# Performance work log

Measured on AMD Instinct MI355X. Metric: run time of the kernel, lower is better.

## Reference

```python
import jax, jax.numpy as jnp
import numpy as np

B, S, D = 2, 2048, 2048
H, HKV, HD = 32, 8, 64
G = H // HKV  # num_key_value_groups


def setup_inputs() -> dict:
    key = jax.random.key(0)
    ks = jax.random.split(key, 9)
    sc = 0.02
    return {
        "x": jax.random.normal(ks[0], (B, S, D), jnp.float32),
        "wq": jax.random.normal(ks[1], (H * HD, D), jnp.float32) * sc,
        "bq": jax.random.normal(ks[2], (H * HD,), jnp.float32) * sc,
        "wk": jax.random.normal(ks[3], (HKV * HD, D), jnp.float32) * sc,
        "bk": jax.random.normal(ks[4], (HKV * HD,), jnp.float32) * sc,
        "wv": jax.random.normal(ks[5], (HKV * HD, D), jnp.float32) * sc,
        "bv": jax.random.normal(ks[6], (HKV * HD,), jnp.float32) * sc,
        "wo": jax.random.normal(ks[7], (D, H * HD), jnp.float32) * sc,
        "bo": jax.random.normal(ks[8], (D,), jnp.float32) * sc,
    }


def reference(x, wq, bq, wk, bk, wv, bv, wo, bo):
    b, s, _ = x.shape
    # fused-QKV-style projections (nn.Linear: x @ W.T + b)
    q = (jnp.einsum("bsd,ed->bse", x, wq) + bq).reshape(b, s, H, HD)
    k = (jnp.einsum("bsd,ed->bse", x, wk) + bk).reshape(b, s, HKV, HD)
    v = (jnp.einsum("bsd,ed->bse", x, wv) + bv).reshape(b, s, HKV, HD)
    # (B, Hkv, G, S, hd): grouped query heads share a KV head — same math as
    # repeat_kv (expand+flatten) without materializing the expanded KV tensor
    q = q.transpose(0, 2, 1, 3).reshape(b, HKV, G, s, HD)
    k = k.transpose(0, 2, 1, 3)  # (B, Hkv, S, hd)
    v = v.transpose(0, 2, 1, 3)
    scale = 1.0 / jnp.sqrt(jnp.asarray(HD, x.dtype))
    scores = jnp.einsum("bkgqd,bktd->bkgqt", q, k) * scale  # (B,Hkv,G,S,S)
    causal = jnp.tril(jnp.ones((s, s), bool))
    scores = jnp.where(causal, scores, jnp.asarray(-jnp.inf, scores.dtype))
    probs = jax.nn.softmax(scores, axis=-1)
    o = jnp.einsum("bkgqt,bktd->bkgqd", probs, v)  # (B,Hkv,G,S,hd)
    o = o.reshape(b, H, s, HD).transpose(0, 2, 1, 3).reshape(b, s, H * HD)
    return jnp.einsum("bse,de->bsd", o, wo) + bo
```

## Files before the change

kernel.cpp:

```cpp
#include <hip/hip_runtime.h>
#include <hip/hip_bf16.h>
#include <cmath>

#define B_   2
#define S_   2048
#define D_   2048
#define H_   32
#define HKV_ 8
#define HD_  64

using bf16 = __hip_bfloat16;
typedef __bf16    bf16x8 __attribute__((ext_vector_type(8)));
typedef float     floatx4 __attribute__((ext_vector_type(4)));
typedef _Float16  half4 __attribute__((ext_vector_type(4)));

#if __has_builtin(__builtin_amdgcn_exp2f)
#define EXP2(x) __builtin_amdgcn_exp2f(x)
#else
#define EXP2(x) exp2f(x)
#endif

#define QSCALE 0.18033688011112042f

__device__ inline void async16(const void* g, void* l) {
  __builtin_amdgcn_global_load_lds(
      (const __attribute__((address_space(1))) void*)g,
      (__attribute__((address_space(3))) void*)l, 16, 0, 0);
}

#define MFMA32B(a, b, c) __builtin_amdgcn_mfma_f32_16x16x32_bf16((a), (b), (c), 0, 0, 0)
#define MFMA16H(a, b, c) __builtin_amdgcn_mfma_f32_16x16x16f16((a), (b), (c), 0, 0, 0)

__global__ void f2b_all(const float* __restrict__ x,  const float* __restrict__ wq,
                        const float* __restrict__ wk, const float* __restrict__ wv,
                        const float* __restrict__ wo,
                        bf16* __restrict__ xb,  bf16* __restrict__ wqb,
                        bf16* __restrict__ wkb, bf16* __restrict__ wvb,
                        bf16* __restrict__ wob) {
  const int i = blockIdx.x * blockDim.x + threadIdx.x;
  const float* src; bf16* dst; int off; float scale = 1.0f;
  if (i < 1048576)      { src = x;  dst = xb;  off = 0; }
  else if (i < 1572864) { src = wq; dst = wqb; off = 1048576; scale = QSCALE; }
  else if (i < 1703936) { src = wk; dst = wkb; off = 1572864; }
  else if (i < 1835008) { src = wv; dst = wvb; off = 1703936; }
  else                  { src = wo; dst = wob; off = 1835008; }
  const int j = i - off;
  float4 a  = ((const float4*)src)[2 * j];
  float4 b2 = ((const float4*)src)[2 * j + 1];
  alignas(16) bf16 t[8];
  t[0] = __float2bfloat16(a.x * scale);  t[1] = __float2bfloat16(a.y * scale);
  t[2] = __float2bfloat16(a.z * scale);  t[3] = __float2bfloat16(a.w * scale);
  t[4] = __float2bfloat16(b2.x * scale); t[5] = __float2bfloat16(b2.y * scale);
  t[6] = __float2bfloat16(b2.z * scale); t[7] = __float2bfloat16(b2.w * scale);
  ((uint4*)dst)[j] = *(const uint4*)t;
}

template <int MODE, typename OutT>
__device__ inline void gemm_body(const bf16* __restrict__ Ag, const bf16* __restrict__ Bg,
                                 const float* __restrict__ bias, float bscale,
                                 OutT* __restrict__ C, int Ncol, int K, int bm, int colb,
                                 bf16* As, bf16* Bs) {
  const int tid  = threadIdx.x;
  const int wid  = tid >> 6, lane = tid & 63;
  const int lm   = lane & 15, quad = lane >> 4;
  const int wm   = (wid >> 1) * 64, wn = (wid & 1) * 64;

  floatx4 acc[4][4] = {};

  const int l0 = tid * 8;
  const int r0 = l0 >> 5, c0 = l0 & 31;
  const int r1 = r0 + 64;

  for (int k0 = 0; k0 < K; k0 += 32) {
    async16(Ag + (size_t)r0 * K + k0 + c0, &As[l0]);
    async16(Ag + (size_t)r1 * K + k0 + c0, &As[l0 + 2048]);
    async16(Bg + (size_t)r0 * K + k0 + c0, &Bs[l0]);
    async16(Bg + (size_t)r1 * K + k0 + c0, &Bs[l0 + 2048]);
    asm volatile("s_waitcnt vmcnt(0)" ::: "memory");
    __syncthreads();

    bf16x8 aF[4], bF[4];
#pragma unroll
    for (int mi = 0; mi < 4; ++mi)
      aF[mi] = *(const bf16x8*)&As[(wm + mi * 16 + lm) * 32 + quad * 8];
#pragma unroll
    for (int ni = 0; ni < 4; ++ni)
      bF[ni] = *(const bf16x8*)&Bs[(wn + ni * 16 + lm) * 32 + quad * 8];
#pragma unroll
    for (int mi = 0; mi < 4; ++mi)
#pragma unroll
      for (int ni = 0; ni < 4; ++ni) {
        if constexpr (MODE == 2)
          acc[mi][ni] = MFMA32B(aF[mi], bF[ni], acc[mi][ni]);
        else
          acc[mi][ni] = MFMA32B(bF[ni], aF[mi], acc[mi][ni]);
      }
    __syncthreads();
  }

  if constexpr (MODE != 2) {
#pragma unroll
    for (int mi = 0; mi < 4; ++mi) {
      const int row = bm * 128 + wm + mi * 16 + lm;
#pragma unroll
      for (int ni = 0; ni < 4; ++ni) {
        const int col0 = colb + wn + ni * 16 + quad * 4;
        float4 bv4 = *(const float4*)&bias[col0];
        if constexpr (MODE == 0) {
          alignas(8) bf16 t4[4];
#pragma unroll
          for (int r = 0; r < 4; ++r)
            t4[r] = __float2bfloat16(acc[mi][ni][r] + ((const float*)&bv4)[r] * bscale);
          *(uint2*)&((bf16*)C)[(size_t)row * Ncol + col0] = *(const uint2*)t4;
        } else {
          float4 o4;
          o4.x = acc[mi][ni][0] + bv4.x; o4.y = acc[mi][ni][1] + bv4.y;
          o4.z = acc[mi][ni][2] + bv4.z; o4.w = acc[mi][ni][3] + bv4.w;
          *(float4*)&((float*)C)[(size_t)row * Ncol + col0] = o4;
        }
      }
    }
  } else {
#pragma unroll
    for (int mi = 0; mi < 4; ++mi) {
      const int rowg = bm * 128 + wm + mi * 16 + quad * 4;
      const int b    = rowg >> 11, s = rowg & 2047;
      const int tile = s >> 6, kvin = s & 63;
      const int kc = kvin >> 4, qd = (kvin >> 2) & 3;
#pragma unroll
      for (int ni = 0; ni < 4; ++ni) {
        const int col = colb + wn + ni * 16 + lm;
        const float bv = bias[col];
        const int kvh = col >> 6, hd = col & 63;
        const int nh = hd >> 4, lmw = hd & 15;
        const size_t base = ((size_t)((b * 8 + kvh) * 32 + tile) << 12) +
                            (((kc * 4 + nh) * 4 + qd) << 6) + (lmw << 2);
        alignas(8) _Float16 t4[4];
#pragma unroll
        for (int r = 0; r < 4; ++r)
          t4[r] = (_Float16)(acc[mi][ni][r] + bv);
        *(uint2*)&((_Float16*)C)[base] = *(const uint2*)t4;
      }
    }
  }
}

__global__ __launch_bounds__(256, 2)
void gemm_qkv(const bf16* __restrict__ xb,
              const bf16* __restrict__ wq, const bf16* __restrict__ wk,
              const bf16* __restrict__ wv,
              const float* __restrict__ bq, const float* __restrict__ bk,
              const float* __restrict__ bv,
              bf16* __restrict__ Qo, bf16* __restrict__ Ko, _Float16* __restrict__ VG) {
  __shared__ bf16 As[128 * 32];
  __shared__ bf16 Bs[128 * 32];
  const int bn = blockIdx.x, bm = blockIdx.y;
  const int K = D_;
  if (bn < 16) {
    gemm_body<0, bf16>(xb + (size_t)bm * 128 * K, wq + (size_t)(bn * 128) * K, bq, QSCALE,
                       Qo, H_ * HD_, K, bm, bn * 128, As, Bs);
  } else if (bn < 20) {
    gemm_body<0, bf16>(xb + (size_t)bm * 128 * K, wk + (size_t)((bn - 16) * 128) * K, bk, 1.0f,
                       Ko, HKV_ * HD_, K, bm, (bn - 16) * 128, As, Bs);
  } else {
    gemm_body<2, _Float16>(xb + (size_t)bm * 128 * K, wv + (size_t)((bn - 20) * 128) * K, bv, 1.0f,
                           VG, HKV_ * HD_, K, bm, (bn - 20) * 128, As, Bs);
  }
}

__global__ __launch_bounds__(256, 2)
void gemm_o(const bf16* __restrict__ A, const bf16* __restrict__ Bm,
            const float* __restrict__ bias, float* __restrict__ C,
            int Ncol, int K) {
  __shared__ bf16 As[128 * 32];
  __shared__ bf16 Bs[128 * 32];
  const int bn = blockIdx.x, bm = blockIdx.y;
  gemm_body<1, float>(A + (size_t)bm * 128 * K, Bm + (size_t)bn * 128 * K, bias, 1.0f,
                      C, Ncol, K, bm, bn * 128, As, Bs);
}

__global__ __launch_bounds__(256, 4)
void attn_kernel(const bf16* __restrict__ Q, const bf16* __restrict__ K,
                 const _Float16* __restrict__ VG, bf16* __restrict__ O) {
  const int tid = threadIdx.x;
  const int wid = tid >> 6, lane = tid & 63;
  const int lm = lane & 15, quad = lane >> 4;

  const int n   = blockIdx.y * 64 + blockIdx.x;
  const int x3  = n & 7, b1 = (n >> 3) & 1;
  const int pair = n >> 4;
  const int grp  = x3 * 2 + b1;
  const int b    = grp >> 3, kvh = grp & 7;
  const int head = kvh * 4 + wid;

  const int hi = 127 - pair, lo = pair;
  const int nt_hi = (hi >> 2) + 1;
  const int nt_lo = (lo >> 2) + 1;

  __shared__ bf16     Ks[2 * 64 * 64];
  __shared__ _Float16 Vs[2 * 64 * 64];

  const int tb[2] = {hi * 16, lo * 16};

  bf16x8 qf[2][2];
#pragma unroll
  for (int tt = 0; tt < 2; ++tt) {
    const size_t qg = ((size_t)(b * S_ + tb[tt] + lm)) * (H_ * HD_) + head * HD_;
#pragma unroll
    for (int kf = 0; kf < 2; ++kf)
      qf[tt][kf] = *(const bf16x8*)&Q[qg + kf * 32 + quad * 8];
  }

  half4 onesh;
#pragma unroll
  for (int j = 0; j < 4; ++j) onesh[j] = (_Float16)1.0f;

  floatx4 o_acc[2][4] = {};
  floatx4 lacc[2] = {};

  const int tr = tid >> 2;
  const int tc = (tid & 3) * 8;

  auto stage = [&](int t, int buf) {
#pragma unroll
    for (int c = 0; c < 2; ++c) {
      async16(&K[(size_t)(b * S_ + t * 64 + tr) * (HKV_ * HD_) + kvh * HD_ + c * 32 + tc],
              &Ks[buf * 4096 + c * 2048 + tid * 8]);
      async16(&VG[((size_t)(grp * 32 + t) << 12) + c * 2048 + tid * 8],
              &Vs[buf * 4096 + c * 2048 + tid * 8]);
    }
  };

  stage(0, 0);

  for (int t = 0; t < nt_hi; ++t) {
    const int cur = t & 1;
    asm volatile("s_waitcnt vmcnt(0)" ::: "memory");
    __syncthreads();
    if (t + 1 < nt_hi) stage(t + 1, cur ^ 1);

    const bf16*     Kb = &Ks[cur * 4096];
    const _Float16* Vb = &Vs[cur * 4096];
    const int t0 = t * 64;
    const int nact = (t < nt_lo) ? 2 : 1;

    int kcmax[2], kcross[2];
#pragma unroll
    for (int tt = 0; tt < 2; ++tt) {
      const int rel = tb[tt] + 15 - t0;
      kcmax[tt]  = (tt < nact) ? ((rel >> 4) >= 3 ? 4 : (rel >> 4) + 1) : 0;
      kcross[tt] = rel >> 4;
    }

    half4 pb[2][4];
#pragma unroll
    for (int kc = 0; kc < 4; ++kc) {
      if (kc >= kcmax[0]) break;
      bf16x8 kb0 = *(const bf16x8*)&Kb[(kc * 16 + lm) * 32 + quad * 8];
      bf16x8 kb1 = *(const bf16x8*)&Kb[2048 + (kc * 16 + lm) * 32 + quad * 8];
#pragma unroll
      for (int tt = 0; tt < 2; ++tt) {
        if (kc >= kcmax[tt]) continue;
        floatx4 sT = {};
        sT = MFMA32B(kb0, qf[tt][0], sT);
        sT = MFMA32B(kb1, qf[tt][1], sT);
        half4 pk;
        if (kc == kcross[tt]) {
          const int qrel = tb[tt] + lm - t0;
#pragma unroll
          for (int r = 0; r < 4; ++r) {
            float p = (kc * 16 + quad * 4 + r > qrel) ? 0.f : EXP2(sT[r]);
            pk[r] = (_Float16)p;
          }
        } else {
#pragma unroll
          for (int r = 0; r < 4; ++r) pk[r] = (_Float16)EXP2(sT[r]);
        }
        pb[tt][kc] = pk;
      }
    }

#pragma unroll
    for (int tt = 0; tt < 2; ++tt) {
      if (kcmax[tt] == 0) continue;
      half4 ps = pb[tt][0];
      if (kcmax[tt] > 1) ps += pb[tt][1];
      if (kcmax[tt] > 2) ps += pb[tt][2];
      if (kcmax[tt] > 3) ps += pb[tt][3];
      lacc[tt] = MFMA16H(onesh, ps, lacc[tt]);
    }

#pragma unroll
    for (int kc = 0; kc < 4; ++kc) {
      if (kc >= kcmax[0]) break;
#pragma unroll
      for (int nh = 0; nh < 4; ++nh) {
        half4 va = *(const half4*)&Vb[((kc * 4 + nh) * 4 + quad) * 64 + lm * 4];
#pragma unroll
        for (int tt = 0; tt < 2; ++tt)
          if (kc < kcmax[tt]) o_acc[tt][nh] = MFMA16H(va, pb[tt][kc], o_acc[tt][nh]);
      }
    }
  }

#pragma unroll
  for (int tt = 0; tt < 2; ++tt) {
    const float rl = 1.f / lacc[tt][0];
    const size_t rowg = (size_t)(b * S_ + tb[tt] + lm);
#pragma unroll
    for (int nh = 0; nh < 4; ++nh) {
      alignas(8) bf16 tmp[4];
#pragma unroll
      for (int r = 0; r < 4; ++r)
        tmp[r] = __float2bfloat16(o_acc[tt][nh][r] * rl);
      *(uint2*)&O[rowg * (H_ * HD_) + head * HD_ + nh * 16 + quad * 4] = *(uint2*)tmp;
    }
  }
}

extern "C" void kernel_launch(void* const* d_in, const int* in_sizes, int n_in,
                              void* d_out, int out_size, void* d_ws, size_t ws_size,
                              hipStream_t stream) {
  (void)in_sizes; (void)n_in; (void)out_size; (void)ws_size;
  const float* x  = (const float*)d_in[0];
  const float* wq = (const float*)d_in[1];
  const float* bq = (const float*)d_in[2];
  const float* wk = (const float*)d_in[3];
  const float* bk = (const float*)d_in[4];
  const float* wv = (const float*)d_in[5];
  const float* bv = (const float*)d_in[6];
  const float* wo = (const float*)d_in[7];
  const float* bo = (const float*)d_in[8];
  float* out = (float*)d_out;

  const int M = B_ * S_;
  const int E = H_ * HD_;
  const int EKV = HKV_ * HD_;

  char* ws = (char*)d_ws;
  size_t off = 0;
  auto alloc = [&](size_t bytes) {
    char* p = ws + off;
    off += (bytes + 255) & ~(size_t)255;
    return p;
  };
  bf16* xb  = (bf16*)alloc((size_t)M * D_ * 2);
  bf16* wqb = (bf16*)alloc((size_t)E * D_ * 2);
  bf16* wkb = (bf16*)alloc((size_t)EKV * D_ * 2);
  bf16* wvb = (bf16*)alloc((size_t)EKV * D_ * 2);
  bf16* wob = (bf16*)alloc((size_t)D_ * E * 2);
  bf16* Qb  = (bf16*)alloc((size_t)M * E * 2);
  bf16* Kb  = (bf16*)alloc((size_t)M * EKV * 2);
  _Float16* VG = (_Float16*)alloc((size_t)M * EKV * 2);
  bf16* Ob  = (bf16*)alloc((size_t)M * E * 2);

  f2b_all<<<9216, 256, 0, stream>>>(x, wq, wk, wv, wo, xb, wqb, wkb, wvb, wob);

  gemm_qkv<<<dim3(24, M / 128), 256, 0, stream>>>(xb, wqb, wkb, wvb, bq, bk, bv,
                                                  Qb, Kb, VG);

  attn_kernel<<<dim3(64, 16), 256, 0, stream>>>(Qb, Kb, VG, Ob);

  gemm_o<<<dim3(D_ / 128, M / 128), 256, 0, stream>>>(Ob, wob, bo, out, D_, D_);
}
```

Measured before the change: 294.4 us.

## Replace QKV GEMM with 256x256-tile, 8-wave, double-buffered pipelined kernel

The QKV projection GEMM moves from 128x128 tiles with a single-stage LDS load to a new 512-thread kernel using 256x256 tiles and 64-wide K steps. Global-to-LDS async loads for the next tiles are double-buffered and interleaved with the MFMA phases, LDS columns are XOR-swizzled, and s_setprio raises priority around the MFMA blocks. Blocks are remapped with a swizzle to improve L2 reuse. The intent is to hide memory latency and raise arithmetic intensity. The costs are much higher register and LDS pressure (128KB LDS) and tight hand-counted vmcnt waits that must stay correct.

```diff
diff --git a/kernel.cpp b/kernel.cpp
--- a/kernel.cpp
+++ b/kernel.cpp
@@ -90,81 +90,23 @@
     for (int mi = 0; mi < 4; ++mi)
 #pragma unroll
       for (int ni = 0; ni < 4; ++ni) {
-        if constexpr (MODE == 2)
-          acc[mi][ni] = MFMA32B(aF[mi], bF[ni], acc[mi][ni]);
-        else
-          acc[mi][ni] = MFMA32B(bF[ni], aF[mi], acc[mi][ni]);
+        acc[mi][ni] = MFMA32B(bF[ni], aF[mi], acc[mi][ni]);
       }
     __syncthreads();
   }
 
-  if constexpr (MODE != 2) {
-#pragma unroll
-    for (int mi = 0; mi < 4; ++mi) {
-      const int row = bm * 128 + wm + mi * 16 + lm;
-#pragma unroll
-      for (int ni = 0; ni < 4; ++ni) {
-        const int col0 = colb + wn + ni * 16 + quad * 4;
-        float4 bv4 = *(const float4*)&bias[col0];
-        if constexpr (MODE == 0) {
-          alignas(8) bf16 t4[4];
-#pragma unroll
-          for (int r = 0; r < 4; ++r)
-            t4[r] = __float2bfloat16(acc[mi][ni][r] + ((const float*)&bv4)[r] * bscale);
-          *(uint2*)&((bf16*)C)[(size_t)row * Ncol + col0] = *(const uint2*)t4;
-        } else {
-          float4 o4;
-          o4.x = acc[mi][ni][0] + bv4.x; o4.y = acc[mi][ni][1] + bv4.y;
-          o4.z = acc[mi][ni][2] + bv4.z; o4.w = acc[mi][ni][3] + bv4.w;
-          *(float4*)&((float*)C)[(size_t)row * Ncol + col0] = o4;
-        }
-      }
-    }
-  } else {
-#pragma unroll
-    for (int mi = 0; mi < 4; ++mi) {
-      const int rowg = bm * 128 + wm + mi * 16 + quad * 4;
-      const int b    = rowg >> 11, s = rowg & 2047;
-      const int tile = s >> 6, kvin = s & 63;
-      const int kc = kvin >> 4, qd = (kvin >> 2) & 3;
-#pragma unroll
-      for (int ni = 0; ni < 4; ++ni) {
-        const int col = colb + wn + ni * 16 + lm;
-        const float bv = bias[col];
-        const int kvh = col >> 6, hd = col & 63;
-        const int nh = hd >> 4, lmw = hd & 15;
-        const size_t base = ((size_t)((b * 8 + kvh) * 32 + tile) << 12) +
-                            (((kc * 4 + nh) * 4 + qd) << 6) + (lmw << 2);
-        alignas(8) _Float16 t4[4];
-#pragma unroll
-        for (int r = 0; r < 4; ++r)
-          t4[r] = (_Float16)(acc[mi][ni][r] + bv);
-        *(uint2*)&((_Float16*)C)[base] = *(const uint2*)t4;
-      }
-    }
-  }
-}
-
-__global__ __launch_bounds__(256, 2)
-void gemm_qkv(const bf16* __restrict__ xb,
-              const bf16* __restrict__ wq, const bf16* __restrict__ wk,
-              const bf16* __restrict__ wv,
-              const float* __restrict__ bq, const float* __restrict__ bk,
-              const float* __restrict__ bv,
-              bf16* __restrict__ Qo, bf16* __restrict__ Ko, _Float16* __restrict__ VG) {
-  __shared__ bf16 As[128 * 32];
-  __shared__ bf16 Bs[128 * 32];
-  const int bn = blockIdx.x, bm = blockIdx.y;
-  const int K = D_;
-  if (bn < 16) {
-    gemm_body<0, bf16>(xb + (size_t)bm * 128 * K, wq + (size_t)(bn * 128) * K, bq, QSCALE,
-                       Qo, H_ * HD_, K, bm, bn * 128, As, Bs);
-  } else if (bn < 20) {
-    gemm_body<0, bf16>(xb + (size_t)bm * 128 * K, wk + (size_t)((bn - 16) * 128) * K, bk, 1.0f,
-                       Ko, HKV_ * HD_, K, bm, (bn - 16) * 128, As, Bs);
-  } else {
-    gemm_body<2, _Float16>(xb + (size_t)bm * 128 * K, wv + (size_t)((bn - 20) * 128) * K, bv, 1.0f,
-                           VG, HKV_ * HD_, K, bm, (bn - 20) * 128, As, Bs);
+#pragma unroll
+  for (int mi = 0; mi < 4; ++mi) {
+    const int row = bm * 128 + wm + mi * 16 + lm;
+#pragma unroll
+    for (int ni = 0; ni < 4; ++ni) {
+      const int col0 = colb + wn + ni * 16 + quad * 4;
+      float4 bv4 = *(const float4*)&bias[col0];
+      float4 o4;
+      o4.x = acc[mi][ni][0] + bv4.x; o4.y = acc[mi][ni][1] + bv4.y;
+      o4.z = acc[mi][ni][2] + bv4.z; o4.w = acc[mi][ni][3] + bv4.w;
+      *(float4*)&((float*)C)[(size_t)row * Ncol + col0] = o4;
+    }
   }
 }
 
@@ -177,6 +119,195 @@
   const int bn = blockIdx.x, bm = blockIdx.y;
   gemm_body<1, float>(A + (size_t)bm * 128 * K, Bm + (size_t)bn * 128 * K, bias, 1.0f,
                       C, Ncol, K, bm, bn * 128, As, Bs);
+}
+
+template <int MODE>
+__device__ __forceinline__ void qkv8_body(
+    const bf16* __restrict__ Ag, const bf16* __restrict__ Bg,
+    const float* __restrict__ bias, float bscale,
+    bf16* __restrict__ outB, _Float16* __restrict__ outV,
+    int Ncol, int colb, int bm, bf16* L) {
+  constexpr int NT = D_ / 64;
+  const int tid = threadIdx.x;
+  const int wid = tid >> 6, lane = tid & 63;
+  const int lm = lane & 15, quad = lane >> 4;
+  const int wm = wid >> 2, wn = wid & 3;
+
+  const int cOff = (quad * 8) ^ (((lm >> 3) & 1) << 4);
+  const bf16* LA0 = L + (wm * 128 + lm) * 32 + cOff;
+  const bf16* LB0 = L + 8192 + (wn * 64 + lm) * 32 + cOff;
+
+  const int r0 = tid >> 2;
+  const int csrc = ((tid & 3) * 8) ^ (((tid >> 5) & 1) << 4);
+  const bf16* Asrc = Ag + (size_t)r0 * D_ + csrc;
+  const bf16* Bsrc = Bg + (size_t)r0 * D_ + csrc;
+  bf16* Ld = L + tid * 8;
+
+  floatx4 acc[8][4] = {};
+
+#define BARX() { asm volatile("" ::: "memory"); __builtin_amdgcn_s_barrier(); \
+                 asm volatile("" ::: "memory"); }
+#define LGKM0() asm volatile("s_waitcnt lgkmcnt(0)" ::: "memory")
+#define STG_A(tt, kk, DB) { const size_t ko = (size_t)(tt) * 64 + (kk) * 32;   \
+    async16(Asrc + ko,                   (DB) + (kk) * 16384);                 \
+    async16(Asrc + ko + (size_t)128 * D_, (DB) + (kk) * 16384 + 4096); }
+#define STG_B(tt, kk, DB) { const size_t ko = (size_t)(tt) * 64 + (kk) * 32;   \
+    async16(Bsrc + ko,                   (DB) + 8192 + (kk) * 16384);          \
+    async16(Bsrc + ko + (size_t)128 * D_, (DB) + 8192 + (kk) * 16384 + 4096); }
+
+  STG_A(0, 0, Ld); STG_B(0, 0, Ld); STG_A(0, 1, Ld); STG_B(0, 1, Ld);
+  STG_A(1, 0, Ld + 32768); STG_B(1, 0, Ld + 32768);
+  asm volatile("s_waitcnt vmcnt(8)" ::: "memory");
+  BARX();
+
+  auto tile = [&](int t, const int BUF) __attribute__((always_inline)) {
+    const bf16* LA = LA0 + BUF;
+    const bf16* LB = LB0 + BUF;
+    bf16* SD  = Ld + BUF;
+    bf16* SDo = Ld + (BUF ^ 32768);
+    const bool s1 = (t + 1) < NT, s2 = (t + 2) < NT;
+    bf16x8 aF[4], bF[4];
+
+#pragma unroll
+    for (int i = 0; i < 4; ++i) aF[i] = *(const bf16x8*)(LA + i * 512);
+#pragma unroll
+    for (int i = 0; i < 4; ++i) bF[i] = *(const bf16x8*)(LB + i * 512);
+    if (s1) STG_A(t + 1, 1, SDo);
+    BARX(); LGKM0();
+    __builtin_amdgcn_s_setprio(1);
+#pragma unroll
+    for (int mi = 0; mi < 4; ++mi)
+#pragma unroll
+      for (int ni = 0; ni < 4; ++ni) {
+        if constexpr (MODE == 2) acc[mi][ni] = MFMA32B(aF[mi], bF[ni], acc[mi][ni]);
+        else                     acc[mi][ni] = MFMA32B(bF[ni], aF[mi], acc[mi][ni]);
+      }
+    __builtin_amdgcn_s_setprio(0);
+    BARX();
+
+#pragma unroll
+    for (int i = 0; i < 4; ++i) aF[i] = *(const bf16x8*)(LA + (i + 4) * 512);
+    if (s1) STG_B(t + 1, 1, SDo);
+    BARX(); LGKM0();
+    __builtin_amdgcn_s_setprio(1);
+#pragma unroll
+    for (int mi = 0; mi < 4; ++mi)
+#pragma unroll
+      for (int ni = 0; ni < 4; ++ni) {
+        if constexpr (MODE == 2) acc[mi + 4][ni] = MFMA32B(aF[mi], bF[ni], acc[mi + 4][ni]);
+        else                     acc[mi + 4][ni] = MFMA32B(bF[ni], aF[mi], acc[mi + 4][ni]);
+      }
+    __builtin_amdgcn_s_setprio(0);
+    if (s1) { asm volatile("s_waitcnt vmcnt(8)" ::: "memory"); }
+    else    { asm volatile("s_waitcnt vmcnt(0)" ::: "memory"); }
+    BARX();
+
+#pragma unroll
+    for (int i = 0; i < 4; ++i) aF[i] = *(const bf16x8*)(LA + 16384 + i * 512);
+#pragma unroll
+    for (int i = 0; i < 4; ++i) bF[i] = *(const bf16x8*)(LB + 16384 + i * 512);
+    if (s2) STG_A(t + 2, 0, SD);
+    BARX(); LGKM0();
+    __builtin_amdgcn_s_setprio(1);
+#pragma unroll
+    for (int mi = 0; mi < 4; ++mi)
+#pragma unroll
+      for (int ni = 0; ni < 4; ++ni) {
+        if constexpr (MODE == 2) acc[mi][ni] = MFMA32B(aF[mi], bF[ni], acc[mi][ni]);
+        else                     acc[mi][ni] = MFMA32B(bF[ni], aF[mi], acc[mi][ni]);
+      }
+    __builtin_amdgcn_s_setprio(0);
+    BARX();
+
+#pragma unroll
+    for (int i = 0; i < 4; ++i) aF[i] = *(const bf16x8*)(LA + 16384 + (i + 4) * 512);
+    if (s2) STG_B(t + 2, 0, SD);
+    BARX(); LGKM0();
+    __builtin_amdgcn_s_setprio(1);
+#pragma unroll
+    for (int mi = 0; mi < 4; ++mi)
+#pragma unroll
+      for (int ni = 0; ni < 4; ++ni) {
+        if constexpr (MODE == 2) acc[mi + 4][ni] = MFMA32B(aF[mi], bF[ni], acc[mi + 4][ni]);
+        else                     acc[mi + 4][ni] = MFMA32B(bF[ni], aF[mi], acc[mi + 4][ni]);
+      }
+    __builtin_amdgcn_s_setprio(0);
+    if (s2)      { asm volatile("s_waitcnt vmcnt(8)" ::: "memory"); }
+    else if (s1) { asm volatile("s_waitcnt vmcnt(4)" ::: "memory"); }
+    BARX();
+  };
+
+  for (int t = 0; t < NT; t += 2) { tile(t, 0); tile(t + 1, 32768); }
+
+#undef BARX
+#undef LGKM0
+#undef STG_A
+#undef STG_B
+
+  const int rowb = bm * 256 + wm * 128;
+  if constexpr (MODE == 0) {
+#pragma unroll
+    for (int mi = 0; mi < 8; ++mi) {
+      const int row = rowb + mi * 16 + lm;
+#pragma unroll
+      for (int ni = 0; ni < 4; ++ni) {
+        const int col0 = colb + wn * 64 + ni * 16 + quad * 4;
+        float4 bv4 = *(const float4*)&bias[col0];
+        alignas(8) bf16 t4[4];
+#pragma unroll
+        for (int r = 0; r < 4; ++r)
+          t4[r] = __float2bfloat16(acc[mi][ni][r] + ((const float*)&bv4)[r] * bscale);
+        *(uint2*)&outB[(size_t)row * Ncol + col0] = *(const uint2*)t4;
+      }
+    }
+  } else {
+#pragma unroll
+    for (int mi = 0; mi < 8; ++mi) {
+      const int rowg = rowb + mi * 16 + quad * 4;
+      const int b    = rowg >> 11, s = rowg & 2047;
+      const int tl   = s >> 6, kvin = s & 63;
+      const int kc   = kvin >> 4, qd = (kvin >> 2) & 3;
+#pragma unroll
+      for (int ni = 0; ni < 4; ++ni) {
+        const int col = colb + wn * 64 + ni * 16 + lm;
+        const float bv = bias[col];
+        const int kvh = col >> 6, hd = col & 63;
+        const int nh = hd >> 4, lmw = hd & 15;
+        const size_t base = ((size_t)((b * 8 + kvh) * 32 + tl) << 12) +
+                            (((kc * 4 + nh) * 4 + qd) << 6) + (lmw << 2);
+        alignas(8) _Float16 t4[4];
+#pragma unroll
+        for (int r = 0; r < 4; ++r)
+          t4[r] = (_Float16)(acc[mi][ni][r] + bv);
+        *(uint2*)&outV[base] = *(const uint2*)t4;
+      }
+    }
+  }
+}
+
+__global__ __launch_bounds__(512, 2)
+void gemm_qkv8(const bf16* __restrict__ xb,
+               const bf16* __restrict__ wq, const bf16* __restrict__ wk,
+               const bf16* __restrict__ wv,
+               const float* __restrict__ bq, const float* __restrict__ bk,
+               const float* __restrict__ bv,
+               bf16* __restrict__ Qo, bf16* __restrict__ Ko,
+               _Float16* __restrict__ VG) {
+  __shared__ bf16 L[65536];
+  const int id  = blockIdx.x;
+  const int swz = (id & 7) * 24 + (id >> 3);
+  const int bm  = swz / 12, bn = swz % 12;
+  const bf16* Ag = xb + (size_t)bm * 256 * D_;
+  if (bn < 8) {
+    qkv8_body<0>(Ag, wq + (size_t)bn * 256 * D_, bq, QSCALE, Qo, nullptr,
+                 H_ * HD_, bn * 256, bm, L);
+  } else if (bn < 10) {
+    qkv8_body<0>(Ag, wk + (size_t)(bn - 8) * 256 * D_, bk, 1.0f, Ko, nullptr,
+                 HKV_ * HD_, (bn - 8) * 256, bm, L);
+  } else {
+    qkv8_body<2>(Ag, wv + (size_t)(bn - 10) * 256 * D_, bv, 1.0f, nullptr, VG,
+                 HKV_ * HD_, (bn - 10) * 256, bm, L);
+  }
 }
 
 __global__ __launch_bounds__(256, 4)
@@ -356,8 +487,8 @@
 
   f2b_all<<<9216, 256, 0, stream>>>(x, wq, wk, wv, wo, xb, wqb, wkb, wvb, wob);
 
-  gemm_qkv<<<dim3(24, M / 128), 256, 0, stream>>>(xb, wqb, wkb, wvb, bq, bk, bv,
-                                                  Qb, Kb, VG);
+  gemm_qkv8<<<dim3(192), dim3(512), 0, stream>>>(xb, wqb, wkb, wvb, bq, bk, bv,
+                                                 Qb, Kb, VG);
 
   attn_kernel<<<dim3(64, 16), 256, 0, stream>>>(Qb, Kb, VG, Ob);
 
```

Result: slower. 303.2 us (+3.0%).
